# Kernel tuning notes

Hardware: AMD Instinct MI355X
Metric: run time of the kernel (lower is better)

The kernel has to match this reference:

```python
import jax, jax.numpy as jnp
import numpy as np

VOCAB, EMBED, CONT, HID = 829, 8, 40, 32
B, T, CODES = 2048, 256, 32
IN_DIM = EMBED + CONT + 1  # 49: embedding-sum + continuous feats + vanco feedback
SCALE = 1000.0  # all four regularizer scales


def setup_inputs() -> dict:
    key = jax.random.key(0)
    ks = jax.random.split(key, 14)
    s = 1.0 / np.sqrt(HID)
    return {
        "cont": jax.random.normal(ks[0], (B, T, CONT), jnp.float32),
        "cat": jax.random.randint(ks[1], (B, T, CODES), 0, VOCAB),
        "lb": jax.random.uniform(ks[2], (B, T), jnp.float32),
        "dose": jax.random.uniform(ks[3], (B, T), jnp.float32),
        "td": jax.random.uniform(ks[4], (B, T), jnp.float32),
        "v_from_weight": jax.random.uniform(ks[5], (B, T), jnp.float32) + 0.5,
        "vanco_el": jax.random.uniform(ks[6], (B, T), jnp.float32),
        "embed": jax.random.normal(ks[7], (VOCAB, EMBED), jnp.float32) * 0.02,
        "W_ih": jax.random.uniform(ks[8], (3 * HID, IN_DIM), jnp.float32, -s, s),
        "W_hh": jax.random.uniform(ks[9], (3 * HID, HID), jnp.float32, -s, s),
        "b_ih": jax.random.uniform(ks[10], (3 * HID,), jnp.float32, -s, s),
        "b_hh": jax.random.uniform(ks[11], (3 * HID,), jnp.float32, -s, s),
        "W_out": jax.random.uniform(ks[12], (2, HID), jnp.float32, -s, s),
        "b_out": jax.random.uniform(ks[13], (2,), jnp.float32, -s, s),
    }


def _gru_cell(x, h, W_ih, W_hh, b_ih, b_hh):
    gi = x @ W_ih.T + b_ih  # [B, 3H]
    gh = h @ W_hh.T + b_hh
    i_r, i_z, i_n = jnp.split(gi, 3, axis=1)
    h_r, h_z, h_n = jnp.split(gh, 3, axis=1)
    r = jax.nn.sigmoid(i_r + h_r)
    z = jax.nn.sigmoid(i_z + h_z)
    n = jnp.tanh(i_n + r * h_n)
    return (1.0 - z) * n + z * h


def reference(cont, cat, lb, dose, td, v_from_weight, vanco_el,
              embed, W_ih, W_hh, b_ih, b_hh, W_out, b_out):
    dt = cont.dtype
    mask = (lb != 0).astype(dt)  # [B, T]
    # EHR embedding: sum code embeddings per step, concat continuous features
    out_emb = jnp.concatenate([embed[cat].sum(axis=2), cont], axis=2)  # [B, T, 48]
    Bn, Tn = lb.shape
    # feedback uses previous step's mask/label (zeros at step 0)
    fm = jnp.concatenate([jnp.zeros((Bn, 1), dt), mask[:, :-1]], axis=1)
    fl = jnp.concatenate([jnp.zeros((Bn, 1), dt), lb[:, :-1]], axis=1)

    def step(carry, xs):
        h, tm, prev_concn = carry
        e_t, fm_t, fl_t, d_t, td_t = xs
        vfb = jax.lax.stop_gradient(prev_concn) * (1.0 - fm_t) + fl_t * fm_t
        x = jnp.concatenate([e_t, vfb[:, None]], axis=1)  # [B, 49]
        h2 = _gru_cell(x, h, W_ih, W_hh, b_ih, b_hh)
        kv = jnp.exp(h2 @ W_out.T + b_out)  # [B, 2]
        k, v = kv[:, 0], kv[:, 1]
        A = jnp.exp(-k * td_t)
        Bq = (1.0 / k) * (1.0 - jnp.exp(-k * d_t)) * jnp.exp(-k * (td_t - d_t))
        tm2 = tm * A + Bq
        concn = tm2 / (v + 1e-6)
        return (h2, tm2, concn), (concn, k, v)

    init = (jnp.zeros((Bn, HID), dt), jnp.zeros((Bn,), dt), jnp.zeros((Bn,), dt))
    xs = (out_emb.transpose(1, 0, 2), fm.T, fl.T, dose.T, td.T)
    _, (concn, K, V) = jax.lax.scan(step, init, xs)
    output, K, V = concn.T, K.T, V.T  # [B, T]

    kv_change = ((K[:, 1:] - K[:, :-1]) ** 2).mean() * SCALE \
              + ((V[:, 1:] - V[:, :-1]) ** 2).mean() * SCALE
    mse_loss = (((output - lb) * mask) ** 2).sum() / mask.sum()
    K0, V0 = vanco_el[:, 0], v_from_weight[:, 0]
    loss = mse_loss + ((K0 - K[:, 0]) ** 2).mean() * SCALE \
                    + ((V0 - V[:, 0]) ** 2).mean() * SCALE + kv_change
    return (K, V, output, loss, mse_loss)
```

## Files before the change

kernel.cpp:

```cpp
#include <hip/hip_runtime.h>


constexpr int Bn = 2048, Tn = 256;
constexpr int HID = 32, CONT = 40, EMB = 8;
constexpr int VOCAB = 829, CODES = 32;
constexpr int BT = Bn * Tn;
constexpr int LOSS_BLOCKS = 256;

typedef float f32x2 __attribute__((ext_vector_type(2)));

__device__ __forceinline__ float frcp(float x) { return __builtin_amdgcn_rcpf(x); }

__device__ __forceinline__ float swap_add(float x) {
  return x + __shfl_xor(x, 32, 64);
}

template <int CTRL>
__device__ __forceinline__ float dpp_add(float x) {
  int y = __builtin_amdgcn_update_dpp(0, __float_as_int(x), CTRL, 0xf, 0xf, true);
  return x + __int_as_float(y);
}

__global__ __launch_bounds__(256, 2) void rnn_kernel(
    const float* __restrict__ cont, const int* __restrict__ cat,
    const float* __restrict__ lb, const float* __restrict__ dose,
    const float* __restrict__ tdp, const float* __restrict__ embed,
    const float* __restrict__ W_ih, const float* __restrict__ W_hh,
    const float* __restrict__ b_ih, const float* __restrict__ b_hh,
    const float* __restrict__ W_out, const float* __restrict__ b_out,
    float* __restrict__ out) {
  __shared__ __attribute__((aligned(16))) float esh[VOCAB * EMB];
  __shared__ __attribute__((aligned(16))) float ebl[4][64][EMB];
  __shared__ __attribute__((aligned(16))) float hsh[4][HID];

  const int tid = threadIdx.x;
  const int wv = tid >> 6;
  const int j = tid & 63;
  const int u = j & 31;
  const int half = j >> 5;
  const int b = blockIdx.x * 4 + wv;
  const int base = b * Tn;

  for (int i = tid; i < VOCAB * EMB; i += 256) esh[i] = embed[i];
  __syncthreads();

  f32x2 wxr2[12], wxz2[12], wxn2[12];
  {
    float tr[24], tz[24], tn_[24];
    const float* Wr = W_ih + (size_t)u * 49;
    const float* Wz = W_ih + (size_t)(HID + u) * 49;
    const float* Wn = W_ih + (size_t)(2 * HID + u) * 49;
    const int eo = half * 4;
    const int co = 8 + half * 20;
#pragma unroll
    for (int k = 0; k < 4; k++) { tr[k] = Wr[eo + k]; tz[k] = Wz[eo + k]; tn_[k] = Wn[eo + k]; }
#pragma unroll
    for (int k = 0; k < 20; k++) {
      tr[4 + k] = Wr[co + k]; tz[4 + k] = Wz[co + k]; tn_[4 + k] = Wn[co + k];
    }
#pragma unroll
    for (int k = 0; k < 12; k++) {
      wxr2[k] = (f32x2){tr[2 * k], tr[2 * k + 1]};
      wxz2[k] = (f32x2){tz[2 * k], tz[2 * k + 1]};
      wxn2[k] = (f32x2){tn_[2 * k], tn_[2 * k + 1]};
    }
  }
  const float wvr = half ? W_ih[(size_t)u * 49 + 48] : 0.0f;
  const float wvz = half ? W_ih[(size_t)(HID + u) * 49 + 48] : 0.0f;
  const float wvn = half ? W_ih[(size_t)(2 * HID + u) * 49 + 48] : 0.0f;
  f32x2 whr2[8], whz2[8], whn2[8];
#pragma unroll
  for (int k = 0; k < 8; k++) {
    whr2[k] = (f32x2){W_hh[(size_t)u * HID + half * 16 + 2 * k],
                      W_hh[(size_t)u * HID + half * 16 + 2 * k + 1]};
    whz2[k] = (f32x2){W_hh[(size_t)(HID + u) * HID + half * 16 + 2 * k],
                      W_hh[(size_t)(HID + u) * HID + half * 16 + 2 * k + 1]};
    whn2[k] = (f32x2){W_hh[(size_t)(2 * HID + u) * HID + half * 16 + 2 * k],
                      W_hh[(size_t)(2 * HID + u) * HID + half * 16 + 2 * k + 1]};
  }
  const float br = half ? 0.0f : (b_ih[u] + b_hh[u]);
  const float bz = half ? 0.0f : (b_ih[HID + u] + b_hh[HID + u]);
  const float bni = half ? 0.0f : b_ih[2 * HID + u];
  const float bnh = half ? 0.0f : b_hh[2 * HID + u];
  const float wkv = W_out[half * HID + u];
  const float bo0 = b_out[0], bo1 = b_out[1];

  hsh[wv][u] = 0.0f;
  float hj = 0.0f, tm = 0.0f, concn = 0.0f;
  float td_c = tdp[base], d_c = dose[base], lbp_c = 0.0f;

  float4 xA[5], xB[5];
  {
    const float4* c4 = reinterpret_cast<const float4*>(cont + (size_t)base * CONT + half * 20);
#pragma unroll
    for (int q = 0; q < 5; q++) xA[q] = c4[q];
  }

#define STEP(XC, XN, TT)                                                          \
  {                                                                               \
    const int t = (TT);                                                           \
    const int tn = (t + 1 < Tn) ? (t + 1) : t;                                    \
                                  \
    const float4 e = *reinterpret_cast<const float4*>(&ebl[wv][t & 63][half * 4]);\
    const float4* h4 = reinterpret_cast<const float4*>(&hsh[wv][half * 16]);      \
    const float4 hv0 = h4[0];                                                     \
    const float4 hv1 = h4[1];                                                     \
    const float4 hv2 = h4[2];                                                     \
    const float4 hv3 = h4[3];                                                     \
                                               \
    { const float4* c4 = reinterpret_cast<const float4*>(                         \
          cont + (size_t)(base + tn) * CONT + half * 20);                         \
      _Pragma("unroll") for (int q = 0; q < 5; q++) XN[q] = c4[q]; }              \
    const float td_n = tdp[base + tn];                                            \
    const float d_n = dose[base + tn];                                            \
    const float lbp_n = lb[base + tn - 1];                                        \
                                     \
    f32x2 arv, azv, anv;                                                          \
    {                                                                             \
      const f32x2 e01 = (f32x2){e.x, e.y}, e23 = (f32x2){e.z, e.w};               \
      arv = wxr2[0] * e01 + wxr2[1] * e23;                                        \
      azv = wxz2[0] * e01 + wxz2[1] * e23;                                        \
      anv = wxn2[0] * e01 + wxn2[1] * e23;                                        \
      _Pragma("unroll") for (int q = 0; q < 5; q++) {                             \
        const float4 xv = XC[q];                                                  \
        const f32x2 x01 = (f32x2){xv.x, xv.y}, x23 = (f32x2){xv.z, xv.w};         \
        arv += wxr2[2 + 2 * q] * x01; arv += wxr2[3 + 2 * q] * x23;               \
        azv += wxz2[2 + 2 * q] * x01; azv += wxz2[3 + 2 * q] * x23;               \
        anv += wxn2[2 + 2 * q] * x01; anv += wxn2[3 + 2 * q] * x23;               \
      }                                                                           \
    }                                                                             \
                                                    \
    f32x2 grv, gzv, gnv;                                                          \
    {                                                                             \
      const f32x2 h01 = (f32x2){hv0.x, hv0.y}, h23 = (f32x2){hv0.z, hv0.w};       \
      const f32x2 h45 = (f32x2){hv1.x, hv1.y}, h67 = (f32x2){hv1.z, hv1.w};       \
      const f32x2 h89 = (f32x2){hv2.x, hv2.y}, hab = (f32x2){hv2.z, hv2.w};       \
      const f32x2 hcd = (f32x2){hv3.x, hv3.y}, hef = (f32x2){hv3.z, hv3.w};       \
      grv = whr2[0] * h01 + whr2[1] * h23;                                        \
      gzv = whz2[0] * h01 + whz2[1] * h23;                                        \
      gnv = whn2[0] * h01 + whn2[1] * h23;                                        \
      grv += whr2[2] * h45; grv += whr2[3] * h67;                                 \
      gzv += whz2[2] * h45; gzv += whz2[3] * h67;                                 \
      gnv += whn2[2] * h45; gnv += whn2[3] * h67;                                 \
      grv += whr2[4] * h89; grv += whr2[5] * hab;                                 \
      gzv += whz2[4] * h89; gzv += whz2[5] * hab;                                 \
      gnv += whn2[4] * h89; gnv += whn2[5] * hab;                                 \
      grv += whr2[6] * hcd; grv += whr2[7] * hef;                                 \
      gzv += whz2[6] * hcd; gzv += whz2[7] * hef;                                 \
      gnv += whn2[6] * hcd; gnv += whn2[7] * hef;                                 \
    }                                                                             \
    const float fmv = (lbp_c != 0.0f) ? 1.0f : 0.0f;                              \
    const float vfb = concn * (1.0f - fmv) + lbp_c * fmv;                         \
    const float ar = arv.x + arv.y + vfb * wvr;                                   \
    const float az = azv.x + azv.y + vfb * wvz;                                   \
    const float an = anv.x + anv.y + vfb * wvn;                                   \
    const float gr = grv.x + grv.y;                                               \
    const float gz = gzv.x + gzv.y;                                               \
    const float gn = gnv.x + gnv.y;                                               \
    const float sr = swap_add(ar + gr + br);                                      \
    const float sz = swap_add(az + gz + bz);                                      \
    const float sa = swap_add(an + bni);                                          \
    const float sg = swap_add(gn + bnh);                                          \
    const float r = frcp(1.0f + __expf(-sr));                                     \
    const float z = frcp(1.0f + __expf(-sz));                                     \
    const float pre = sa + r * sg;                                                \
    const float nv = 1.0f - 2.0f * frcp(__expf(2.0f * pre) + 1.0f);               \
    const float h2 = (1.0f - z) * nv + z * hj;                                    \
    hsh[wv][u] = h2;                                                              \
    hj = h2;                                                                      \
                          \
    float s = h2 * wkv;                                                           \
    s = dpp_add<0x111>(s);                                         \
    s = dpp_add<0x112>(s);                                         \
    s = dpp_add<0x114>(s);                                         \
    s = dpp_add<0x118>(s);                                         \
    s = dpp_add<0x142>(s);  \
    const float pk_s = __int_as_float(__builtin_amdgcn_readlane(__float_as_int(s), 31)); \
    const float pv_s = __int_as_float(__builtin_amdgcn_readlane(__float_as_int(s), 63)); \
    const float kk = __expf(pk_s + bo0);                                          \
    const float vv = __expf(pv_s + bo1);                                          \
    const float Aa = __expf(-kk * td_c);                                          \
    const float eD = __expf(-kk * d_c);                                           \
    const float Bq = frcp(kk) * (1.0f - eD) * __expf(-kk * (td_c - d_c));         \
    tm = tm * Aa + Bq;                                                            \
    concn = tm * frcp(vv + 1e-6f);                                                \
    if (j < 3) {                                                                  \
      const float val = (j == 0) ? kk : ((j == 1) ? vv : concn);                  \
      out[j * BT + base + t] = val;                                               \
    }                                                                             \
    td_c = td_n;                                                                  \
    d_c = d_n;                                                                    \
    lbp_c = lbp_n;                                                                \
  }

  for (int ch = 0; ch < Tn / 64; ++ch) {
    {
      const int4* cp4 =
          reinterpret_cast<const int4*>(cat + ((size_t)(base + ch * 64 + j)) * CODES);
      float a0 = 0.f, a1 = 0.f, a2 = 0.f, a3 = 0.f;
      float a4 = 0.f, a5 = 0.f, a6 = 0.f, a7 = 0.f;
#pragma unroll
      for (int q = 0; q < 8; q++) {
        const int4 c4 = cp4[q];
        {
          const float4* er = reinterpret_cast<const float4*>(esh + c4.x * EMB);
          const float4 r0 = er[0], r1 = er[1];
          a0 += r0.x; a1 += r0.y; a2 += r0.z; a3 += r0.w;
          a4 += r1.x; a5 += r1.y; a6 += r1.z; a7 += r1.w;
        }
        {
          const float4* er = reinterpret_cast<const float4*>(esh + c4.y * EMB);
          const float4 r0 = er[0], r1 = er[1];
          a0 += r0.x; a1 += r0.y; a2 += r0.z; a3 += r0.w;
          a4 += r1.x; a5 += r1.y; a6 += r1.z; a7 += r1.w;
        }
        {
          const float4* er = reinterpret_cast<const float4*>(esh + c4.z * EMB);
          const float4 r0 = er[0], r1 = er[1];
          a0 += r0.x; a1 += r0.y; a2 += r0.z; a3 += r0.w;
          a4 += r1.x; a5 += r1.y; a6 += r1.z; a7 += r1.w;
        }
        {
          const float4* er = reinterpret_cast<const float4*>(esh + c4.w * EMB);
          const float4 r0 = er[0], r1 = er[1];
          a0 += r0.x; a1 += r0.y; a2 += r0.z; a3 += r0.w;
          a4 += r1.x; a5 += r1.y; a6 += r1.z; a7 += r1.w;
        }
      }
      *reinterpret_cast<float4*>(&ebl[wv][j][0]) = make_float4(a0, a1, a2, a3);
      *reinterpret_cast<float4*>(&ebl[wv][j][4]) = make_float4(a4, a5, a6, a7);
    }
    __syncthreads();
#pragma unroll 1
    for (int tl = 0; tl < 64; tl += 2) {
      STEP(xA, xB, ch * 64 + tl);
      STEP(xB, xA, ch * 64 + tl + 1);
    }
  }
#undef STEP
}

__global__ __launch_bounds__(256) void loss_partial_kernel(
    const float* __restrict__ out, const float* __restrict__ lb,
    const float* __restrict__ vel, const float* __restrict__ vfw,
    float* __restrict__ part) {
  float mseN = 0.f, cnt = 0.f, k0 = 0.f, v0 = 0.f, dk = 0.f, dv = 0.f;
  for (int i = blockIdx.x * 256 + threadIdx.x; i < BT; i += LOSS_BLOCKS * 256) {
    const int t = i & (Tn - 1);
    const float l = lb[i];
    const float m = (l != 0.0f) ? 1.0f : 0.0f;
    const float c = out[2 * BT + i];
    const float d = (c - l) * m;
    mseN += d * d;
    cnt += m;
    const float kc = out[i];
    const float vc = out[BT + i];
    if (t > 0) {
      const float kp = out[i - 1];
      const float vp = out[BT + i - 1];
      dk += (kc - kp) * (kc - kp);
      dv += (vc - vp) * (vc - vp);
    } else {
      const float a = vel[i] - kc;
      const float bb = vfw[i] - vc;
      k0 += a * a;
      v0 += bb * bb;
    }
  }
  float acc[6] = {mseN, cnt, k0, v0, dk, dv};
#pragma unroll
  for (int q = 0; q < 6; q++) {
#pragma unroll
    for (int mm = 1; mm < 64; mm <<= 1) acc[q] += __shfl_xor(acc[q], mm, 64);
  }
  __shared__ float red[4][6];
  if ((threadIdx.x & 63) == 0) {
#pragma unroll
    for (int q = 0; q < 6; q++) red[threadIdx.x >> 6][q] = acc[q];
  }
  __syncthreads();
  if (threadIdx.x == 0) {
#pragma unroll
    for (int q = 0; q < 6; q++)
      part[blockIdx.x * 6 + q] = red[0][q] + red[1][q] + red[2][q] + red[3][q];
  }
}

__device__ __forceinline__ void finalize_loss(const float s[6], float* out) {
  const float mse = s[0] / s[1];
  const float loss = mse + (s[2] / (float)Bn) * 1000.0f + (s[3] / (float)Bn) * 1000.0f +
                     (s[4] / (float)(Bn * (Tn - 1))) * 1000.0f +
                     (s[5] / (float)(Bn * (Tn - 1))) * 1000.0f;
  out[3 * BT] = loss;
  out[3 * BT + 1] = mse;
}

__global__ __launch_bounds__(256) void loss_final_kernel(const float* __restrict__ part,
                                                         float* __restrict__ out) {
  float acc[6] = {0.f, 0.f, 0.f, 0.f, 0.f, 0.f};
  for (int i = threadIdx.x; i < LOSS_BLOCKS; i += 256) {
#pragma unroll
    for (int q = 0; q < 6; q++) acc[q] += part[i * 6 + q];
  }
#pragma unroll
  for (int q = 0; q < 6; q++) {
#pragma unroll
    for (int mm = 1; mm < 64; mm <<= 1) acc[q] += __shfl_xor(acc[q], mm, 64);
  }
  __shared__ float red[4][6];
  if ((threadIdx.x & 63) == 0) {
#pragma unroll
    for (int q = 0; q < 6; q++) red[threadIdx.x >> 6][q] = acc[q];
  }
  __syncthreads();
  if (threadIdx.x == 0) {
    float s[6];
#pragma unroll
    for (int q = 0; q < 6; q++) s[q] = red[0][q] + red[1][q] + red[2][q] + red[3][q];
    finalize_loss(s, out);
  }
}

__global__ __launch_bounds__(1024) void loss_single_kernel(
    const float* __restrict__ out, const float* __restrict__ lb,
    const float* __restrict__ vel, const float* __restrict__ vfw,
    float* __restrict__ outw) {
  float mseN = 0.f, cnt = 0.f, k0 = 0.f, v0 = 0.f, dk = 0.f, dv = 0.f;
  for (int i = threadIdx.x; i < BT; i += 1024) {
    const int t = i & (Tn - 1);
    const float l = lb[i];
    const float m = (l != 0.0f) ? 1.0f : 0.0f;
    const float c = out[2 * BT + i];
    const float d = (c - l) * m;
    mseN += d * d;
    cnt += m;
    const float kc = out[i];
    const float vc = out[BT + i];
    if (t > 0) {
      const float kp = out[i - 1];
      const float vp = out[BT + i - 1];
      dk += (kc - kp) * (kc - kp);
      dv += (vc - vp) * (vc - vp);
    } else {
      const float a = vel[i] - kc;
      const float bb = vfw[i] - vc;
      k0 += a * a;
      v0 += bb * bb;
    }
  }
  float acc[6] = {mseN, cnt, k0, v0, dk, dv};
#pragma unroll
  for (int q = 0; q < 6; q++) {
#pragma unroll
    for (int mm = 1; mm < 64; mm <<= 1) acc[q] += __shfl_xor(acc[q], mm, 64);
  }
  __shared__ float red[16][6];
  if ((threadIdx.x & 63) == 0) {
#pragma unroll
    for (int q = 0; q < 6; q++) red[threadIdx.x >> 6][q] = acc[q];
  }
  __syncthreads();
  if (threadIdx.x == 0) {
    float s[6] = {0.f, 0.f, 0.f, 0.f, 0.f, 0.f};
    for (int w = 0; w < 16; w++)
#pragma unroll
      for (int q = 0; q < 6; q++) s[q] += red[w][q];
    finalize_loss(s, outw);
  }
}

extern "C" void kernel_launch(void* const* d_in, const int* in_sizes, int n_in,
                              void* d_out, int out_size, void* d_ws, size_t ws_size,
                              hipStream_t stream) {
  (void)in_sizes; (void)n_in; (void)out_size;
  const float* cont = (const float*)d_in[0];
  const int* cat = (const int*)d_in[1];
  const float* lb = (const float*)d_in[2];
  const float* dose = (const float*)d_in[3];
  const float* tdp = (const float*)d_in[4];
  const float* vfw = (const float*)d_in[5];
  const float* vel = (const float*)d_in[6];
  const float* emb = (const float*)d_in[7];
  const float* W_ih = (const float*)d_in[8];
  const float* W_hh = (const float*)d_in[9];
  const float* b_ih = (const float*)d_in[10];
  const float* b_hh = (const float*)d_in[11];
  const float* W_out = (const float*)d_in[12];
  const float* b_out = (const float*)d_in[13];
  float* out = (float*)d_out;

  rnn_kernel<<<Bn / 4, 256, 0, stream>>>(cont, cat, lb, dose, tdp, emb, W_ih, W_hh,
                                         b_ih, b_hh, W_out, b_out, out);

  if (d_ws != nullptr && ws_size >= (size_t)LOSS_BLOCKS * 6 * sizeof(float)) {
    float* part = (float*)d_ws;
    loss_partial_kernel<<<LOSS_BLOCKS, 256, 0, stream>>>(out, lb, vel, vfw, part);
    loss_final_kernel<<<1, 256, 0, stream>>>(part, out);
  } else {
    loss_single_kernel<<<1, 1024, 0, stream>>>(out, lb, vel, vfw, out);
  }
}
```

Baseline: 230.2 us.

## Fuse loss partial sums into the recurrent kernel, drop separate partial pass

Each wavefront now accumulates the MSE, mask count, initial-step and step-to-step K/V regularizer terms during its recurrence. At the end it writes one partial row per batch element to the workspace, so the separate loss_partial kernel that re-read the outputs and labels is removed. The final reduction now sums Bn partial rows instead of 256 block partials. The cost is an extra label load and a few FLOPs in every serial step, plus more register pressure. Whether this runs depends on the workspace holding Bn*6 floats.

```diff
diff --git a/kernel.cpp b/kernel.cpp
--- a/kernel.cpp
+++ b/kernel.cpp
@@ -5,7 +5,6 @@
 constexpr int HID = 32, CONT = 40, EMB = 8;
 constexpr int VOCAB = 829, CODES = 32;
 constexpr int BT = Bn * Tn;
-constexpr int LOSS_BLOCKS = 256;
 
 typedef float f32x2 __attribute__((ext_vector_type(2)));
 
@@ -21,6 +20,7 @@
   return x + __int_as_float(y);
 }
 
+template <bool FUSE>
 __global__ __launch_bounds__(256, 2) void rnn_kernel(
     const float* __restrict__ cont, const int* __restrict__ cat,
     const float* __restrict__ lb, const float* __restrict__ dose,
@@ -28,7 +28,8 @@
     const float* __restrict__ W_ih, const float* __restrict__ W_hh,
     const float* __restrict__ b_ih, const float* __restrict__ b_hh,
     const float* __restrict__ W_out, const float* __restrict__ b_out,
-    float* __restrict__ out) {
+    const float* __restrict__ vel, const float* __restrict__ vfw,
+    float* __restrict__ part, float* __restrict__ out) {
   __shared__ __attribute__((aligned(16))) float esh[VOCAB * EMB];
   __shared__ __attribute__((aligned(16))) float ebl[4][64][EMB];
   __shared__ __attribute__((aligned(16))) float hsh[4][HID];
@@ -88,6 +89,11 @@
   hsh[wv][u] = 0.0f;
   float hj = 0.0f, tm = 0.0f, concn = 0.0f;
   float td_c = tdp[base], d_c = dose[base], lbp_c = 0.0f;
+
+  float lmse = 0.f, lcnt = 0.f, lk0 = 0.f, lv0 = 0.f, ldk = 0.f, ldv = 0.f;
+  float kprev = 0.f, vprev = 0.f;
+  float vel0 = 0.f, vfw0 = 0.f;
+  if (FUSE) { vel0 = vel[base]; vfw0 = vfw[base]; }
 
   float4 xA[5], xB[5];
   {
@@ -188,6 +194,22 @@
       const float val = (j == 0) ? kk : ((j == 1) ? vv : concn);                  \
       out[j * BT + base + t] = val;                                               \
     }                                                                             \
+    if (FUSE) {           \
+      const float l_t = lb[base + t];                                             \
+      const float m = (l_t != 0.0f) ? 1.0f : 0.0f;                                \
+      const float dd = (concn - l_t) * m;                                         \
+      lmse += dd * dd;                                                            \
+      lcnt += m;                                                                  \
+      if (t > 0) {                                                                \
+        ldk += (kk - kprev) * (kk - kprev);                                       \
+        ldv += (vv - vprev) * (vv - vprev);                                       \
+      } else {                                                                    \
+        lk0 = (vel0 - kk) * (vel0 - kk);                                          \
+        lv0 = (vfw0 - vv) * (vfw0 - vv);                                          \
+      }                                                                           \
+      kprev = kk;                                                                 \
+      vprev = vv;                                                                 \
+    }                                                                             \
     td_c = td_n;                                                                  \
     d_c = d_n;                                                                    \
     lbp_c = lbp_n;                                                                \
@@ -238,51 +260,14 @@
     }
   }
 #undef STEP
-}
-
-__global__ __launch_bounds__(256) void loss_partial_kernel(
-    const float* __restrict__ out, const float* __restrict__ lb,
-    const float* __restrict__ vel, const float* __restrict__ vfw,
-    float* __restrict__ part) {
-  float mseN = 0.f, cnt = 0.f, k0 = 0.f, v0 = 0.f, dk = 0.f, dv = 0.f;
-  for (int i = blockIdx.x * 256 + threadIdx.x; i < BT; i += LOSS_BLOCKS * 256) {
-    const int t = i & (Tn - 1);
-    const float l = lb[i];
-    const float m = (l != 0.0f) ? 1.0f : 0.0f;
-    const float c = out[2 * BT + i];
-    const float d = (c - l) * m;
-    mseN += d * d;
-    cnt += m;
-    const float kc = out[i];
-    const float vc = out[BT + i];
-    if (t > 0) {
-      const float kp = out[i - 1];
-      const float vp = out[BT + i - 1];
-      dk += (kc - kp) * (kc - kp);
-      dv += (vc - vp) * (vc - vp);
-    } else {
-      const float a = vel[i] - kc;
-      const float bb = vfw[i] - vc;
-      k0 += a * a;
-      v0 += bb * bb;
-    }
-  }
-  float acc[6] = {mseN, cnt, k0, v0, dk, dv};
-#pragma unroll
-  for (int q = 0; q < 6; q++) {
-#pragma unroll
-    for (int mm = 1; mm < 64; mm <<= 1) acc[q] += __shfl_xor(acc[q], mm, 64);
-  }
-  __shared__ float red[4][6];
-  if ((threadIdx.x & 63) == 0) {
-#pragma unroll
-    for (int q = 0; q < 6; q++) red[threadIdx.x >> 6][q] = acc[q];
-  }
-  __syncthreads();
-  if (threadIdx.x == 0) {
-#pragma unroll
-    for (int q = 0; q < 6; q++)
-      part[blockIdx.x * 6 + q] = red[0][q] + red[1][q] + red[2][q] + red[3][q];
+
+  if (FUSE) {
+    const float v0s = (j == 0) ? lmse
+                    : (j == 1) ? lcnt
+                    : (j == 2) ? lk0
+                    : (j == 3) ? lv0
+                    : (j == 4) ? ldk : ldv;
+    if (j < 6) part[b * 6 + j] = v0s;
   }
 }
 
@@ -295,10 +280,10 @@
   out[3 * BT + 1] = mse;
 }
 
-__global__ __launch_bounds__(256) void loss_final_kernel(const float* __restrict__ part,
-                                                         float* __restrict__ out) {
+__global__ __launch_bounds__(256) void loss_final2_kernel(const float* __restrict__ part,
+                                                          float* __restrict__ out) {
   float acc[6] = {0.f, 0.f, 0.f, 0.f, 0.f, 0.f};
-  for (int i = threadIdx.x; i < LOSS_BLOCKS; i += 256) {
+  for (int i = threadIdx.x; i < Bn; i += 256) {
 #pragma unroll
     for (int q = 0; q < 6; q++) acc[q] += part[i * 6 + q];
   }
@@ -389,14 +374,17 @@
   const float* b_out = (const float*)d_in[13];
   float* out = (float*)d_out;
 
-  rnn_kernel<<<Bn / 4, 256, 0, stream>>>(cont, cat, lb, dose, tdp, emb, W_ih, W_hh,
-                                         b_ih, b_hh, W_out, b_out, out);
-
-  if (d_ws != nullptr && ws_size >= (size_t)LOSS_BLOCKS * 6 * sizeof(float)) {
+  const bool fuse = (d_ws != nullptr) && (ws_size >= (size_t)Bn * 6 * sizeof(float));
+  if (fuse) {
     float* part = (float*)d_ws;
-    loss_partial_kernel<<<LOSS_BLOCKS, 256, 0, stream>>>(out, lb, vel, vfw, part);
-    loss_final_kernel<<<1, 256, 0, stream>>>(part, out);
+    rnn_kernel<true><<<Bn / 4, 256, 0, stream>>>(cont, cat, lb, dose, tdp, emb, W_ih,
+                                                 W_hh, b_ih, b_hh, W_out, b_out, vel,
+                                                 vfw, part, out);
+    loss_final2_kernel<<<1, 256, 0, stream>>>(part, out);
   } else {
+    rnn_kernel<false><<<Bn / 4, 256, 0, stream>>>(cont, cat, lb, dose, tdp, emb, W_ih,
+                                                  W_hh, b_ih, b_hh, W_out, b_out, vel,
+                                                  vfw, nullptr, out);
     loss_single_kernel<<<1, 1024, 0, stream>>>(out, lb, vel, vfw, out);
   }
 }
```

Result: slower. 242.3 us (+5.3%).
